# Kernel tuning notes

Measured on AMD Instinct MI355X. Metric: run time of the kernel, lower is better.

## Reference

```python
import jax, jax.numpy as jnp
import numpy as np

N, E, F, H, G = 50000, 800000, 64, 64, 100

def setup_inputs() -> dict:
    key = jax.random.key(0)
    ks = jax.random.split(key, 12)
    x = jax.random.normal(ks[0], (N, F), dtype=jnp.float32)
    edge_index = jax.random.randint(ks[1], (2, E), 0, N, dtype=jnp.int64)
    batch = jnp.sort(jax.random.randint(ks[2], (N,), 0, G, dtype=jnp.int64))
    s1 = 1.0 / np.sqrt(F); s2 = 1.0 / np.sqrt(H)
    W1 = jax.random.normal(ks[3], (2, F, H), dtype=jnp.float32) * s1
    b1 = jnp.zeros((H,), dtype=jnp.float32)
    W2 = jax.random.normal(ks[4], (2, H, H), dtype=jnp.float32) * s2
    b2 = jnp.zeros((H,), dtype=jnp.float32)
    gamma = jnp.ones((H,), dtype=jnp.float32)
    beta = jnp.zeros((H,), dtype=jnp.float32)
    linW = jax.random.normal(ks[5], (H, 1), dtype=jnp.float32) * s2
    linb = jnp.zeros((1,), dtype=jnp.float32)
    return {"x": x, "edge_index": edge_index, "batch": batch, "W1": W1, "b1": b1,
            "W2": W2, "b2": b2, "gamma": gamma, "beta": beta, "linW": linW, "linb": linb}

def _edge_norm(row, col, n):
    # get_laplacian(sym) + lambda_max=2: Lhat off-diag weight = -d_i^{-1/2} d_j^{-1/2}, diag = 0
    deg = jax.ops.segment_sum(jnp.ones(row.shape[0], jnp.float32), row, num_segments=n)
    dis = jnp.where(deg > 0, deg ** -0.5, 0.0)
    return -dis[row] * dis[col]

def _cheb(x, row, col, w, W, b):
    # K=2: out = T0(Lhat)x @ W0 + T1(Lhat)x @ W1 + b, T1 = Lhat x via scatter-add
    Tx1 = jax.ops.segment_sum(w[:, None] * x[row], col, num_segments=x.shape[0])
    return x @ W[0] + Tx1 @ W[1] + b

def reference(x, edge_index, batch, W1, b1, W2, b2, gamma, beta, linW, linb):
    row, col = edge_index[0], edge_index[1]
    n = x.shape[0]
    w = _edge_norm(row, col, n)
    h = _cheb(x, row, col, w, W1, b1)
    # BatchNorm1d (training-mode batch stats, eps=1e-5)
    mu = jnp.mean(h, axis=0)
    var = jnp.var(h, axis=0)
    h = (h - mu) * jax.lax.rsqrt(var + 1e-5) * gamma + beta
    # LeakyReLU (default slope 0.01)
    h = jnp.where(h >= 0, h, 0.01 * h)
    h = _cheb(h, row, col, w, W2, b2)
    # global_mean_pool over graph ids
    sums = jax.ops.segment_sum(h, batch, num_segments=G)
    cnts = jax.ops.segment_sum(jnp.ones(n, jnp.float32), batch, num_segments=G)
    pooled = sums / jnp.maximum(cnts, 1.0)[:, None]
    # dropout: identity (eval)
    return pooled @ linW + linb
```

## Files before the change

kernel.cpp:

```cpp
#include <hip/hip_runtime.h>

#define HDIM 64
#define BH 128
#define HB8 12800
#define SBINS 12544
#define GR 32


__device__ __forceinline__ int lbound(const int* __restrict__ b, int n, int v) {
    int lo = 0, hi = n;
    while (lo < hi) { int m = (lo + hi) >> 1; if (b[m] < v) lo = m + 1; else hi = m; }
    return lo;
}

__device__ __forceinline__ unsigned short f2bf(float f) {
    unsigned u = __float_as_uint(f);
    unsigned r = u + 0x7FFFu + ((u >> 16) & 1u);
    return (unsigned short)(r >> 16);
}


__global__ __launch_bounds__(256) void k_hist8(const int* __restrict__ row,
                                               const int* __restrict__ col,
                                               unsigned char* __restrict__ cntP,
                                               unsigned char* __restrict__ degP,
                                               int E, int N, int slice) {
    __shared__ unsigned hbin[HB8];
    int blk = blockIdx.x;
    const int* keys = blockIdx.y ? row : col;
    unsigned char* outP = blockIdx.y ? degP : cntP;
    int binsU = (N + 3) >> 2;
    for (int i = threadIdx.x; i < binsU; i += 256) hbin[i] = 0;
    __syncthreads();
    int e0 = blk * slice, e1 = min(e0 + slice, E);
    for (int e = e0 + threadIdx.x; e < e1; e += 256) {
        int c = keys[e];
        atomicAdd(&hbin[c >> 2], 1u << ((c & 3) << 3));
    }
    __syncthreads();
    unsigned* outU = (unsigned*)(outP + (size_t)blk * N);
    for (int i = threadIdx.x; i < binsU; i += 256) outU[i] = hbin[i];
}

__global__ __launch_bounds__(1024) void k_csrmeta(unsigned char* __restrict__ cntP,
                                                  const unsigned char* __restrict__ degP,
                                                  unsigned short* __restrict__ cnt16,
                                                  float* __restrict__ dis,
                                                  int* __restrict__ start,
                                                  int* __restrict__ agg, int N) {
    __shared__ int wsum[16];
    __shared__ int sTotal, sBase;
    int i = blockIdx.x * 1024 + threadIdx.x;
    int lane = threadIdx.x & 63, w = threadIdx.x >> 6;

    int run = 0, d = 0;
    if (i < N) {
        #pragma unroll 4
        for (int b = 0; b < BH; ++b) {
            int v = cntP[(size_t)b * N + i];
            cntP[(size_t)b * N + i] = (unsigned char)run;
            run += v;
        }
        #pragma unroll 4
        for (int b = 0; b < BH; ++b) d += degP[(size_t)b * N + i];
        cnt16[i] = (unsigned short)run;
        dis[i] = d > 0 ? rsqrtf((float)d) : 0.0f;
    }
    int incl = run;
    #pragma unroll
    for (int off = 1; off < 64; off <<= 1) {
        int u = __shfl_up(incl, off, 64);
        if (lane >= off) incl += u;
    }
    if (lane == 63) wsum[w] = incl;
    __syncthreads();
    if (w == 0) {
        int s = (lane < 16) ? wsum[lane] : 0;
        int si = s;
        #pragma unroll
        for (int off = 1; off < 16; off <<= 1) {
            int u = __shfl_up(si, off, 64);
            if (lane >= off) si += u;
        }
        if (lane < 16) wsum[lane] = si - s;
    }
    __syncthreads();
    int excl = incl - run + wsum[w];
    if (threadIdx.x == 1023) sTotal = excl + run;
    __syncthreads();
    if (threadIdx.x == 0)
        __hip_atomic_store(&agg[blockIdx.x], sTotal + 1,
                           __ATOMIC_RELEASE, __HIP_MEMORY_SCOPE_AGENT);
    if (w == 0) {
        int v = 0;
        if (lane < (int)blockIdx.x) {
            int a;
            do {
                a = __hip_atomic_load(&agg[lane], __ATOMIC_ACQUIRE,
                                      __HIP_MEMORY_SCOPE_AGENT);
            } while (a == 0);
            v = a - 1;
        }
        #pragma unroll
        for (int off = 1; off < 64; off <<= 1) v += __shfl_xor(v, off, 64);
        if (lane == 0) sBase = v;
    }
    __syncthreads();
    if (i < N) start[i] = excl + sBase;
}

__global__ __launch_bounds__(256) void k_sortfill(const int* __restrict__ row,
                                                  const int* __restrict__ col,
                                                  const unsigned char* __restrict__ cntP,
                                                  const int* __restrict__ start,
                                                  unsigned short* __restrict__ er,
                                                  int E, int N, int slice) {
    __shared__ int cur[SBINS];
    int blk = blockIdx.x;
    int lo = blockIdx.y * SBINS;
    int span = min(SBINS, N - lo);
    for (int i = threadIdx.x; i < span; i += 256)
        cur[i] = start[lo + i] + (int)cntP[(size_t)blk * N + lo + i];
    __syncthreads();
    int e0 = blk * slice, e1 = min(e0 + slice, E);
    for (int e = e0 + threadIdx.x; e < e1; e += 256) {
        int c = col[e] - lo;
        int rv = row[e];
        if ((unsigned)c < (unsigned)span) {
            int pos = atomicAdd(&cur[c], 1);
            er[pos] = (unsigned short)rv;
        }
    }
}


__global__ __launch_bounds__(512) void k_gemm2(const float* __restrict__ x,
                                               const float* __restrict__ dis,
                                               const float* __restrict__ W1,
                                               const float* __restrict__ b1,
                                               float* __restrict__ z,
                                               unsigned short* __restrict__ y16, int n) {
    __shared__ float xs[GR][HDIM];
    int tid  = threadIdx.x;
    int j    = tid & 63;
    int half = (tid >> 6) & 1;
    int w2   = tid >> 7;
    int base = blockIdx.x * GR;

    const float* Wb = W1 + (half ? HDIM * HDIM : 0);
    float4 wr[16];
    #pragma unroll
    for (int k4 = 0; k4 < 16; ++k4) {
        wr[k4].x = Wb[(k4 * 4 + 0) * HDIM + j];
        wr[k4].y = Wb[(k4 * 4 + 1) * HDIM + j];
        wr[k4].z = Wb[(k4 * 4 + 2) * HDIM + j];
        wr[k4].w = Wb[(k4 * 4 + 3) * HDIM + j];
    }
    float bj = b1[j];

    {
        int v = tid;
        int r = base + (v >> 4);
        int rc = min(r, n - 1);
        int c = (v & 15) * 4;
        ((float4*)xs)[v] = *(const float4*)&x[(size_t)rc * HDIM + c];
    }
    __syncthreads();

    #pragma unroll
    for (int m = 0; m < 8; ++m) {
        int lr = w2 * 8 + m;
        int r = base + lr;
        if (r < n) {
            const float4* rp = (const float4*)xs[lr];
            float a = 0.f;
            #pragma unroll
            for (int k4 = 0; k4 < 16; ++k4) {
                float4 v = rp[k4];
                a = fmaf(v.x, wr[k4].x, a);
                a = fmaf(v.y, wr[k4].y, a);
                a = fmaf(v.z, wr[k4].z, a);
                a = fmaf(v.w, wr[k4].w, a);
            }
            if (half == 0) z[(size_t)r * HDIM + j] = a + bj;
            else           y16[(size_t)r * HDIM + j] = f2bf(dis[r] * a);
        }
    }
}

__global__ __launch_bounds__(256) void k_gatherH(const unsigned short* __restrict__ er,
                                                 const int* __restrict__ start,
                                                 const unsigned short* __restrict__ cnt16,
                                                 const float* __restrict__ dis,
                                                 const unsigned* __restrict__ y32,
                                                 const float* __restrict__ z,
                                                 float* __restrict__ h,
                                                 float* __restrict__ pstat, int n) {
    __shared__ float red[2][4][HDIM];
    int w = threadIdx.x >> 6;
    int lane = threadIdx.x & 63;
    int l  = lane & 31;
    int hi = lane >> 5;
    float sx = 0.f, sy = 0.f, qx = 0.f, qy = 0.f;
    #pragma unroll
    for (int m = 0; m < 4; ++m) {
        int i = blockIdx.x * 16 + w * 4 + m;
        if (i >= n) continue;
        int s = start[i], nd = cnt16[i];
        float a0x = 0.f, a0y = 0.f, a1x = 0.f, a1y = 0.f;
        int k = 0;
        for (; k + 3 < nd; k += 4) {
            int r0 = er[s + k + hi];
            int r1 = er[s + k + 2 + hi];
            unsigned v0 = y32[(size_t)r0 * 32 + l];
            unsigned v1 = y32[(size_t)r1 * 32 + l];
            a0x += __uint_as_float(v0 << 16);
            a0y += __uint_as_float(v0 & 0xFFFF0000u);
            a1x += __uint_as_float(v1 << 16);
            a1y += __uint_as_float(v1 & 0xFFFF0000u);
        }
        for (; k < nd; k += 2) {
            int idx = k + hi;
            if (idx < nd) {
                unsigned v = y32[(size_t)er[s + idx] * 32 + l];
                a0x += __uint_as_float(v << 16);
                a0y += __uint_as_float(v & 0xFFFF0000u);
            }
        }
        float ax = a0x + a1x, ay = a0y + a1y;
        ax += __shfl_xor(ax, 32, 64);
        ay += __shfl_xor(ay, 32, 64);
        if (hi == 0) {
            float di = dis[i];
            float2 zv = *(const float2*)&z[(size_t)i * HDIM + 2 * l];
            float h0 = zv.x - di * ax;
            float h1 = zv.y - di * ay;
            *(float2*)&h[(size_t)i * HDIM + 2 * l] = make_float2(h0, h1);
            sx += h0; sy += h1;
            qx = fmaf(h0, h0, qx); qy = fmaf(h1, h1, qy);
        }
    }
    if (hi == 0) {
        *(float2*)&red[0][w][2 * l] = make_float2(sx, sy);
        *(float2*)&red[1][w][2 * l] = make_float2(qx, qy);
    }
    __syncthreads();
    if (w == 0) {
        int j = lane;
        float s  = red[0][0][j] + red[0][1][j] + red[0][2][j] + red[0][3][j];
        float ss = red[1][0][j] + red[1][1][j] + red[1][2][j] + red[1][3][j];
        pstat[(size_t)blockIdx.x * 128 + j]      = s;
        pstat[(size_t)blockIdx.x * 128 + 64 + j] = ss;
    }
}

__global__ __launch_bounds__(256) void k_statred(const float* __restrict__ pstat,
                                                 float* __restrict__ stats, int nb) {
    int idx = blockIdx.x;
    float s = 0.f;
    for (int b = threadIdx.x; b < nb; b += 256)
        s += pstat[(size_t)b * 128 + idx];
    __shared__ float red[256];
    red[threadIdx.x] = s;
    __syncthreads();
    for (int off = 128; off > 0; off >>= 1) {
        if (threadIdx.x < off) red[threadIdx.x] += red[threadIdx.x + off];
        __syncthreads();
    }
    if (threadIdx.x == 0) stats[idx] = red[0];
}

__global__ void k_prep(const float* __restrict__ stats,
                       const float* __restrict__ gamma, const float* __restrict__ beta,
                       const float* __restrict__ W2, const float* __restrict__ b2,
                       const float* __restrict__ linW, const float* __restrict__ linb,
                       float* __restrict__ scale, float* __restrict__ shift,
                       float* __restrict__ u0, float* __restrict__ u1,
                       float* __restrict__ c0, int n) {
    int k = threadIdx.x;
    if (k >= HDIM) return;
    float inv_n = 1.0f / (float)n;
    float mu  = stats[k] * inv_n;
    float var = stats[64 + k] * inv_n - mu * mu;
    float rs  = rsqrtf(var + 1e-5f);
    float sc  = rs * gamma[k];
    scale[k] = sc;
    shift[k] = beta[k] - mu * sc;
    float a0 = 0.f, a1 = 0.f;
    #pragma unroll 8
    for (int j = 0; j < HDIM; ++j) {
        float lw = linW[j];
        a0 = fmaf(W2[k * HDIM + j], lw, a0);
        a1 = fmaf(W2[HDIM * HDIM + k * HDIM + j], lw, a1);
    }
    u0[k] = a0;
    u1[k] = a1;
    if (k == 0) {
        float c = linb[0];
        for (int j = 0; j < HDIM; ++j) c = fmaf(b2[j], linW[j], c);
        c0[0] = c;
    }
}

__global__ __launch_bounds__(256) void k_node(const float* __restrict__ h,
                                              const float* __restrict__ scale,
                                              const float* __restrict__ shift,
                                              const float* __restrict__ u0,
                                              const float* __restrict__ u1,
                                              const float* __restrict__ dis,
                                              float* __restrict__ a, float* __restrict__ t,
                                              int n) {
    int i = blockIdx.x * 4 + (threadIdx.x >> 6);
    if (i >= n) return;
    int j = threadIdx.x & 63;
    float v = fmaf(h[(size_t)i * HDIM + j], scale[j], shift[j]);
    v = v >= 0.f ? v : 0.01f * v;
    float p0 = v * u0[j];
    float p1 = v * u1[j];
    #pragma unroll
    for (int off = 32; off > 0; off >>= 1) {
        p0 += __shfl_xor(p0, off, 64);
        p1 += __shfl_xor(p1, off, 64);
    }
    if (j == 0) { a[i] = p0; t[i] = dis[i] * p1; }
}

__global__ __launch_bounds__(256) void k_gp(const unsigned short* __restrict__ er,
                                            const int* __restrict__ start,
                                            const unsigned short* __restrict__ cnt16,
                                            const float* __restrict__ dis,
                                            const float* __restrict__ t,
                                            const float* __restrict__ a,
                                            const int* __restrict__ batch,
                                            float* __restrict__ gsum, int n) {
    __shared__ float gacc[16];
    __shared__ int sGmin;
    int tid = threadIdx.x;
    int i = (int)blockIdx.x * 64 + (tid >> 2);
    int q = tid & 3;
    if (tid < 16) gacc[tid] = 0.f;
    if (tid == 0) sGmin = batch[min((int)blockIdx.x * 64, n - 1)];
    __syncthreads();
    if (i < n) {
        int s = start[i], nd = cnt16[i];
        float acc = 0.f;
        int k = q;
        for (; k + 4 < nd; k += 8) {
            acc += t[er[s + k]] + t[er[s + k + 4]];
        }
        if (k < nd) acc += t[er[s + k]];
        acc += __shfl_xor(acc, 1, 4);
        acc += __shfl_xor(acc, 2, 4);
        if (q == 0) {
            float s2 = a[i] - dis[i] * acc;
            int g = batch[i];
            int rel = g - sGmin;
            if ((unsigned)rel < 16u) atomicAdd(&gacc[rel], s2);
            else                     atomicAdd(&gsum[g], s2);
        }
    }
    __syncthreads();
    if (tid < 16 && gacc[tid] != 0.f) atomicAdd(&gsum[sGmin + tid], gacc[tid]);
}

__global__ void k_out(const float* __restrict__ gsum, const int* __restrict__ batch,
                      const float* __restrict__ c0, const float* __restrict__ linb,
                      float* __restrict__ out, int n, int g) {
    int i = blockIdx.x * blockDim.x + threadIdx.x;
    if (i < g) {
        int lo = lbound(batch, n, i);
        int hi = lbound(batch, n, i + 1);
        int c = hi - lo;
        out[i] = c > 0 ? gsum[i] / (float)c + c0[0] : linb[0];
    }
}


extern "C" void kernel_launch(void* const* d_in, const int* in_sizes, int n_in,
                              void* d_out, int out_size, void* d_ws, size_t ws_size,
                              hipStream_t stream) {
    const float* x     = (const float*)d_in[0];
    const int*   eidx  = (const int*)d_in[1];
    const int*   batch = (const int*)d_in[2];
    const float* W1    = (const float*)d_in[3];
    const float* b1    = (const float*)d_in[4];
    const float* W2    = (const float*)d_in[5];
    const float* b2    = (const float*)d_in[6];
    const float* gamma = (const float*)d_in[7];
    const float* beta  = (const float*)d_in[8];
    const float* linW  = (const float*)d_in[9];
    const float* linb  = (const float*)d_in[10];
    float* out = (float*)d_out;

    const int N = in_sizes[0] / HDIM;
    const int E = in_sizes[1] / 2;
    const int G = out_size;
    const int NB = (N + 1023) / 1024;
    const int slice = (E + BH - 1) / BH;
    const int NHB = (N + 15) / 16;

    const int* row = eidx;
    const int* col = eidx + E;

    char* wsb = (char*)d_ws;
    float* h    = (float*)wsb;               wsb += (size_t)N * HDIM * 4;
    unsigned char* cntP = (unsigned char*)h;
    unsigned char* degP = cntP + (size_t)BH * N;
    float* z    = (float*)wsb;               wsb += (size_t)N * HDIM * 4;
    unsigned short* y16 = (unsigned short*)wsb; wsb += (size_t)N * HDIM * 2;
    unsigned short* cnt16 = (unsigned short*)wsb; wsb += (size_t)N * 2;
    unsigned short* er    = (unsigned short*)wsb; wsb += (size_t)E * 2;
    int*   start = (int*)wsb;                wsb += (size_t)N * 4;
    float* dis   = (float*)wsb;              wsb += (size_t)N * 4;
    float* a     = (float*)wsb;              wsb += (size_t)N * 4;
    float* t     = (float*)wsb;              wsb += (size_t)N * 4;
    float* pstat = (float*)wsb;              wsb += (size_t)NHB * 128 * 4;
    int*   agg   = (int*)wsb;                wsb += 64 * 4;
    float* gsum  = (float*)wsb;              wsb += 128 * 4;
    float* stats = (float*)wsb;              wsb += 128 * 4;
    float* scale = (float*)wsb;              wsb += HDIM * 4;
    float* shift = (float*)wsb;              wsb += HDIM * 4;
    float* u0    = (float*)wsb;              wsb += HDIM * 4;
    float* u1    = (float*)wsb;              wsb += HDIM * 4;
    float* c0    = (float*)wsb;              wsb += 64;

    (void)hipMemsetAsync(agg, 0, (64 + 128) * 4, stream);

    k_hist8<<<dim3(BH, 2), 256, 0, stream>>>(row, col, cntP, degP, E, N, slice);
    k_csrmeta<<<NB, 1024, 0, stream>>>(cntP, degP, cnt16, dis, start, agg, N);
    k_sortfill<<<dim3(BH, 4), 256, 0, stream>>>(row, col, cntP, start, er, E, N, slice);
    k_gemm2<<<(N + GR - 1) / GR, 512, 0, stream>>>(x, dis, W1, b1, z, y16, N);
    k_gatherH<<<NHB, 256, 0, stream>>>(er, start, cnt16, dis, (const unsigned*)y16, z,
                                       h, pstat, N);
    k_statred<<<128, 256, 0, stream>>>(pstat, stats, NHB);
    k_prep<<<1, 64, 0, stream>>>(stats, gamma, beta, W2, b2, linW, linb,
                                 scale, shift, u0, u1, c0, N);
    k_node<<<(N + 3) / 4, 256, 0, stream>>>(h, scale, shift, u0, u1, dis, a, t, N);
    k_gp<<<(N + 63) / 64, 256, 0, stream>>>(er, start, cnt16, dis, t, a, batch, gsum, N);
    k_out<<<1, 128, 0, stream>>>(gsum, batch, c0, linb, out, N, G);
}
```

Measured before the change: 177.3 us.

## Store z and h intermediates in bf16; shrink csrmeta blocks to 256 threads

The z output of the first GEMM and the pre-BatchNorm activations h are now stored as bf16 instead of fp32, halving their write and read traffic across k_gemm2, k_gatherH and k_node. The CSR metadata scan now uses 256-thread blocks, so there are about four times as many blocks, each lane summing several predecessor aggregates in the decoupled lookback. cntP and degP get their own workspace regions instead of aliasing h. The cost is bf16 rounding error on intermediates and a longer serial lookback chain across more blocks.

Measured after the change: 178.3 us. About the same (+0.6%).

```diff
diff --git a/kernel.cpp b/kernel.cpp
--- a/kernel.cpp
+++ b/kernel.cpp
@@ -17,6 +17,9 @@
     unsigned u = __float_as_uint(f);
     unsigned r = u + 0x7FFFu + ((u >> 16) & 1u);
     return (unsigned short)(r >> 16);
+}
+__device__ __forceinline__ float bf2f(unsigned short s) {
+    return __uint_as_float((unsigned)s << 16);
 }
 
 
@@ -42,16 +45,18 @@
     for (int i = threadIdx.x; i < binsU; i += 256) outU[i] = hbin[i];
 }
 
-__global__ __launch_bounds__(1024) void k_csrmeta(unsigned char* __restrict__ cntP,
-                                                  const unsigned char* __restrict__ degP,
-                                                  unsigned short* __restrict__ cnt16,
-                                                  float* __restrict__ dis,
-                                                  int* __restrict__ start,
-                                                  int* __restrict__ agg, int N) {
-    __shared__ int wsum[16];
-    __shared__ int sTotal, sBase;
-    int i = blockIdx.x * 1024 + threadIdx.x;
-    int lane = threadIdx.x & 63, w = threadIdx.x >> 6;
+__global__ __launch_bounds__(256) void k_csrmeta(unsigned char* __restrict__ cntP,
+                                                 const unsigned char* __restrict__ degP,
+                                                 unsigned short* __restrict__ cnt16,
+                                                 float* __restrict__ dis,
+                                                 int* __restrict__ start,
+                                                 int* __restrict__ agg, int N) {
+    __shared__ int wsum[4];
+    __shared__ int sBase;
+    int bid = blockIdx.x;
+    int tid = threadIdx.x;
+    int i = bid * 256 + tid;
+    int lane = tid & 63, w = tid >> 6;
 
     int run = 0, d = 0;
     if (i < N) {
@@ -74,32 +79,21 @@
     }
     if (lane == 63) wsum[w] = incl;
     __syncthreads();
-    if (w == 0) {
-        int s = (lane < 16) ? wsum[lane] : 0;
-        int si = s;
-        #pragma unroll
-        for (int off = 1; off < 16; off <<= 1) {
-            int u = __shfl_up(si, off, 64);
-            if (lane >= off) si += u;
-        }
-        if (lane < 16) wsum[lane] = si - s;
-    }
-    __syncthreads();
-    int excl = incl - run + wsum[w];
-    if (threadIdx.x == 1023) sTotal = excl + run;
-    __syncthreads();
-    if (threadIdx.x == 0)
-        __hip_atomic_store(&agg[blockIdx.x], sTotal + 1,
+    int woff = 0;
+    for (int k = 0; k < w; ++k) woff += wsum[k];
+    int excl = incl - run + woff;
+    if (tid == 0)
+        __hip_atomic_store(&agg[bid], wsum[0] + wsum[1] + wsum[2] + wsum[3] + 1,
                            __ATOMIC_RELEASE, __HIP_MEMORY_SCOPE_AGENT);
     if (w == 0) {
         int v = 0;
-        if (lane < (int)blockIdx.x) {
+        for (int b = lane; b < bid; b += 64) {
             int a;
             do {
-                a = __hip_atomic_load(&agg[lane], __ATOMIC_ACQUIRE,
+                a = __hip_atomic_load(&agg[b], __ATOMIC_ACQUIRE,
                                       __HIP_MEMORY_SCOPE_AGENT);
             } while (a == 0);
-            v = a - 1;
+            v += a - 1;
         }
         #pragma unroll
         for (int off = 1; off < 64; off <<= 1) v += __shfl_xor(v, off, 64);
@@ -138,7 +132,7 @@
                                                const float* __restrict__ dis,
                                                const float* __restrict__ W1,
                                                const float* __restrict__ b1,
-                                               float* __restrict__ z,
+                                               unsigned short* __restrict__ z16,
                                                unsigned short* __restrict__ y16, int n) {
     __shared__ float xs[GR][HDIM];
     int tid  = threadIdx.x;
@@ -182,7 +176,7 @@
                 a = fmaf(v.z, wr[k4].z, a);
                 a = fmaf(v.w, wr[k4].w, a);
             }
-            if (half == 0) z[(size_t)r * HDIM + j] = a + bj;
+            if (half == 0) z16[(size_t)r * HDIM + j] = f2bf(a + bj);
             else           y16[(size_t)r * HDIM + j] = f2bf(dis[r] * a);
         }
     }
@@ -193,8 +187,8 @@
                                                  const unsigned short* __restrict__ cnt16,
                                                  const float* __restrict__ dis,
                                                  const unsigned* __restrict__ y32,
-                                                 const float* __restrict__ z,
-                                                 float* __restrict__ h,
+                                                 const unsigned* __restrict__ z32,
+                                                 unsigned* __restrict__ h32,
                                                  float* __restrict__ pstat, int n) {
     __shared__ float red[2][4][HDIM];
     int w = threadIdx.x >> 6;
@@ -232,10 +226,10 @@
         ay += __shfl_xor(ay, 32, 64);
         if (hi == 0) {
             float di = dis[i];
-            float2 zv = *(const float2*)&z[(size_t)i * HDIM + 2 * l];
-            float h0 = zv.x - di * ax;
-            float h1 = zv.y - di * ay;
-            *(float2*)&h[(size_t)i * HDIM + 2 * l] = make_float2(h0, h1);
+            unsigned zv = z32[(size_t)i * 32 + l];
+            float h0 = __uint_as_float(zv << 16) - di * ax;
+            float h1 = __uint_as_float(zv & 0xFFFF0000u) - di * ay;
+            h32[(size_t)i * 32 + l] = (unsigned)f2bf(h0) | ((unsigned)f2bf(h1) << 16);
             sx += h0; sy += h1;
             qx = fmaf(h0, h0, qx); qy = fmaf(h1, h1, qy);
         }
@@ -302,7 +296,7 @@
     }
 }
 
-__global__ __launch_bounds__(256) void k_node(const float* __restrict__ h,
+__global__ __launch_bounds__(256) void k_node(const unsigned short* __restrict__ h16,
                                               const float* __restrict__ scale,
                                               const float* __restrict__ shift,
                                               const float* __restrict__ u0,
@@ -313,7 +307,7 @@
     int i = blockIdx.x * 4 + (threadIdx.x >> 6);
     if (i >= n) return;
     int j = threadIdx.x & 63;
-    float v = fmaf(h[(size_t)i * HDIM + j], scale[j], shift[j]);
+    float v = fmaf(bf2f(h16[(size_t)i * HDIM + j]), scale[j], shift[j]);
     v = v >= 0.f ? v : 0.01f * v;
     float p0 = v * u0[j];
     float p1 = v * u1[j];
@@ -395,7 +389,7 @@
     const int N = in_sizes[0] / HDIM;
     const int E = in_sizes[1] / 2;
     const int G = out_size;
-    const int NB = (N + 1023) / 1024;
+    const int NB = (N + 255) / 256;
     const int slice = (E + BH - 1) / BH;
     const int NHB = (N + 15) / 16;
 
@@ -403,11 +397,11 @@
     const int* col = eidx + E;
 
     char* wsb = (char*)d_ws;
-    float* h    = (float*)wsb;               wsb += (size_t)N * HDIM * 4;
-    unsigned char* cntP = (unsigned char*)h;
-    unsigned char* degP = cntP + (size_t)BH * N;
-    float* z    = (float*)wsb;               wsb += (size_t)N * HDIM * 4;
+    unsigned char* cntP = (unsigned char*)wsb;  wsb += (size_t)BH * N;
+    unsigned char* degP = (unsigned char*)wsb;  wsb += (size_t)BH * N;
+    unsigned short* z16 = (unsigned short*)wsb; wsb += (size_t)N * HDIM * 2;
     unsigned short* y16 = (unsigned short*)wsb; wsb += (size_t)N * HDIM * 2;
+    unsigned short* h16 = (unsigned short*)wsb; wsb += (size_t)N * HDIM * 2;
     unsigned short* cnt16 = (unsigned short*)wsb; wsb += (size_t)N * 2;
     unsigned short* er    = (unsigned short*)wsb; wsb += (size_t)E * 2;
     int*   start = (int*)wsb;                wsb += (size_t)N * 4;
@@ -415,7 +409,7 @@
     float* a     = (float*)wsb;              wsb += (size_t)N * 4;
     float* t     = (float*)wsb;              wsb += (size_t)N * 4;
     float* pstat = (float*)wsb;              wsb += (size_t)NHB * 128 * 4;
-    int*   agg   = (int*)wsb;                wsb += 64 * 4;
+    int*   agg   = (int*)wsb;                wsb += 256 * 4;
     float* gsum  = (float*)wsb;              wsb += 128 * 4;
     float* stats = (float*)wsb;              wsb += 128 * 4;
     float* scale = (float*)wsb;              wsb += HDIM * 4;
@@ -424,18 +418,18 @@
     float* u1    = (float*)wsb;              wsb += HDIM * 4;
     float* c0    = (float*)wsb;              wsb += 64;
 
-    (void)hipMemsetAsync(agg, 0, (64 + 128) * 4, stream);
+    (void)hipMemsetAsync(agg, 0, (256 + 128) * 4, stream);
 
     k_hist8<<<dim3(BH, 2), 256, 0, stream>>>(row, col, cntP, degP, E, N, slice);
-    k_csrmeta<<<NB, 1024, 0, stream>>>(cntP, degP, cnt16, dis, start, agg, N);
+    k_csrmeta<<<NB, 256, 0, stream>>>(cntP, degP, cnt16, dis, start, agg, N);
     k_sortfill<<<dim3(BH, 4), 256, 0, stream>>>(row, col, cntP, start, er, E, N, slice);
-    k_gemm2<<<(N + GR - 1) / GR, 512, 0, stream>>>(x, dis, W1, b1, z, y16, N);
-    k_gatherH<<<NHB, 256, 0, stream>>>(er, start, cnt16, dis, (const unsigned*)y16, z,
-                                       h, pstat, N);
+    k_gemm2<<<(N + GR - 1) / GR, 512, 0, stream>>>(x, dis, W1, b1, z16, y16, N);
+    k_gatherH<<<NHB, 256, 0, stream>>>(er, start, cnt16, dis, (const unsigned*)y16,
+                                       (const unsigned*)z16, (unsigned*)h16, pstat, N);
     k_statred<<<128, 256, 0, stream>>>(pstat, stats, NHB);
     k_prep<<<1, 64, 0, stream>>>(stats, gamma, beta, W2, b2, linW, linb,
                                  scale, shift, u0, u1, c0, N);
-    k_node<<<(N + 3) / 4, 256, 0, stream>>>(h, scale, shift, u0, u1, dis, a, t, N);
+    k_node<<<(N + 3) / 4, 256, 0, stream>>>(h16, scale, shift, u0, u1, dis, a, t, N);
     k_gp<<<(N + 63) / 64, 256, 0, stream>>>(er, start, cnt16, dis, t, a, batch, gsum, N);
     k_out<<<1, 128, 0, stream>>>(gsum, batch, c0, linb, out, N, G);
 }
```
